# Performance work log

Measured on AMD Instinct MI355X. Metric: run time of the kernel, lower is better.

Reference implementation:

```python
import jax, jax.numpy as jnp
import numpy as np

N_TOKENS = 8192
TOP_K = 2
N_EXPERTS = 8
D_MODEL = 1024
D_FF = 2048
CAPACITY = 3072  # static per-expert buffer; mean load 2048, overflow prob ~0
FP8_MAX = 448.0


def setup_inputs() -> dict:
    key = jax.random.key(0)
    ks = jax.random.split(key, 6)
    x = jax.random.normal(ks[0], (N_TOKENS, D_MODEL), dtype=jnp.float32)
    expert_indices = jax.random.randint(ks[1], (N_TOKENS, TOP_K), 0, N_EXPERTS)
    expert_weights = jax.nn.softmax(jax.random.normal(ks[2], (N_TOKENS, TOP_K)), axis=-1).astype(jnp.float32)
    # trunc_normal init, std = sqrt(1/3)/sqrt(fan_in), fan_in = w.shape[1]
    std_in = (1.0 / 3.0) ** 0.5 / D_MODEL ** 0.5
    std_ff = (1.0 / 3.0) ** 0.5 / D_FF ** 0.5
    w1 = jnp.clip(jax.random.normal(ks[3], (N_EXPERTS, D_MODEL, D_FF), jnp.float32) * std_in, -2 * std_in, 2 * std_in)
    w2 = jnp.clip(jax.random.normal(ks[4], (N_EXPERTS, D_MODEL, D_FF), jnp.float32) * std_in, -2 * std_in, 2 * std_in)
    w3 = jnp.clip(jax.random.normal(ks[5], (N_EXPERTS, D_FF, D_MODEL), jnp.float32) * std_ff, -2 * std_ff, 2 * std_ff)
    return {"x": x, "expert_indices": expert_indices, "expert_weights": expert_weights,
            "w1": w1, "w2": w2, "w3": w3}


def reference(x, expert_indices, expert_weights, w1, w2, w3):
    n_tokens, d_model = x.shape
    top_k = expert_indices.shape[1]
    n_experts = w1.shape[0]

    # input fp8 scale (buffer fill_ in torch -> no grad)
    input_scale = jax.lax.stop_gradient(FP8_MAX / (jnp.max(jnp.abs(x)) + 1e-12) * 0.9)
    # w*_scale buffers are ones at inference (recalibration happens only randomly in training)
    w_scale = jnp.float32(1.0)

    # ---- dispatch: stable sort assignments by expert, compute slot positions ----
    flat_experts = expert_indices.reshape(-1)                       # [N*K]
    flat_weights = expert_weights.reshape(-1)                       # [N*K]
    token_indices = jnp.repeat(jnp.arange(n_tokens), top_k)         # [N*K]
    order = jnp.argsort(flat_experts)                               # stable sort
    sorted_experts = flat_experts[order]
    sorted_weights = flat_weights[order]
    sorted_tokens = token_indices[order]
    counts = jnp.bincount(flat_experts, length=n_experts)           # [E]
    seg_starts = jnp.cumsum(counts) - counts                        # [E]
    positions = jnp.arange(n_tokens * top_k) - seg_starts[sorted_experts]

    # scatter tokens into padded per-expert buffers [E, CAP, d]; OOB slots dropped
    padded = jnp.zeros((n_experts, CAPACITY, d_model), x.dtype)
    padded = padded.at[sorted_experts, positions].set(x[sorted_tokens], mode='drop')

    # ---- grouped SwiGLU with fp8-style quant/dequant scaling ----
    inp_scaled = jnp.clip(padded * input_scale, -FP8_MAX, FP8_MAX)  # [E, C, d]
    w1_s = jnp.clip(w1 * w_scale, -FP8_MAX, FP8_MAX)
    w2_s = jnp.clip(w2 * w_scale, -FP8_MAX, FP8_MAX)
    w3_s = jnp.clip(w3 * w_scale, -FP8_MAX, FP8_MAX)
    gate = jnp.einsum('ecd,edf->ecf', inp_scaled, w1_s) / (input_scale * w_scale)
    gate = jax.nn.silu(gate)
    value = jnp.einsum('ecd,edf->ecf', inp_scaled, w2_s) / (input_scale * w_scale)
    hidden = gate * value                                            # [E, C, f]
    # per-expert hidden amax (padded rows are zero -> same max as valid rows)
    hidden_amax = jnp.max(jnp.abs(hidden), axis=(1, 2))              # [E]
    hidden_scale = (FP8_MAX / (hidden_amax + 1e-12) * 0.9)[:, None, None]
    hidden_scaled = jnp.clip(hidden * hidden_scale, -FP8_MAX, FP8_MAX)
    out_padded = jnp.einsum('ecf,efd->ecd', hidden_scaled, w3_s) / (hidden_scale * w_scale)

    # ---- combine: gather per-assignment outputs, weight, scatter-add per token ----
    valid = positions < CAPACITY
    gathered = out_padded[sorted_experts, jnp.minimum(positions, CAPACITY - 1)]
    gathered = gathered * jnp.where(valid, sorted_weights, 0.0)[:, None]
    output = jnp.zeros((n_tokens, d_model), x.dtype).at[sorted_tokens].add(gathered)
    return output
```

## Files before the change

### kernel.cpp

```cpp
#include <hip/hip_runtime.h>

#define N_TOK   8192
#define TOPK    2
#define N_EXP   8
#define DM      1024
#define DFF     2048
#define CAP     3072

typedef __attribute__((ext_vector_type(8))) short bf16x8;
typedef __attribute__((ext_vector_type(4))) float f32x4;

__device__ __forceinline__ unsigned short f2bf(float x) {
    union { float f; unsigned u; } un; un.f = x;
    unsigned r = un.u + 0x7fffu + ((un.u >> 16) & 1u);
    return (unsigned short)(r >> 16);
}

__device__ __forceinline__ void glds16(const void* g, void* l) {
    __builtin_amdgcn_global_load_lds(
        (const __attribute__((address_space(1))) unsigned int*)g,
        (__attribute__((address_space(3))) unsigned int*)l, 16, 0, 0);
}

__global__ void cvt_x_kernel(const float4* __restrict__ x, ushort4* __restrict__ xb) {
    int i = blockIdx.x * 256 + threadIdx.x;
    float4 v = x[i];
    ushort4 o;
    o.x = f2bf(v.x); o.y = f2bf(v.y); o.z = f2bf(v.z); o.w = f2bf(v.w);
    xb[i] = o;
}

__global__ void transpose_cvt_kernel(const float* __restrict__ in, unsigned short* __restrict__ out,
                                     int R, int C) {
    __shared__ float tile[32][33];
    const int e = blockIdx.z;
    const int r0 = blockIdx.y * 32, c0 = blockIdx.x * 32;
    const float* src = in + ((size_t)e * R + r0) * C + c0;
    const int tx = threadIdx.x, ty = threadIdx.y;
#pragma unroll
    for (int i = 0; i < 4; i++)
        tile[ty + 8 * i][tx] = src[(size_t)(ty + 8 * i) * C + tx];
    __syncthreads();
    unsigned short* dst = out + ((size_t)e * C + c0) * R + r0;
#pragma unroll
    for (int i = 0; i < 4; i++) {
        int c = ty + 8 * i;
        dst[(size_t)c * R + tx] = f2bf(tile[tx][c]);
    }
}

__global__ void dispatch_kernel(const int* __restrict__ eidx, const float* __restrict__ ewt,
                                int* __restrict__ counts, int* __restrict__ row_token,
                                float* __restrict__ row_weight) {
    int i = blockIdx.x * 256 + threadIdx.x;
    if (i < N_TOK * TOPK) {
        int e = eidx[i];
        int pos = atomicAdd(&counts[e], 1);
        if (pos < CAP) {
            row_token[e * CAP + pos] = i >> 1;
            row_weight[e * CAP + pos] = ewt[i];
        }
    }
}

__global__ __launch_bounds__(256, 2)
void gemm1_kernel(const unsigned short* __restrict__ xb, const unsigned short* __restrict__ w1t,
                  const unsigned short* __restrict__ w2t, const int* __restrict__ counts,
                  const int* __restrict__ row_token, unsigned short* __restrict__ hidden) {
    const int e = blockIdx.z;
    const int r0 = blockIdx.y * 128;
    if (r0 >= counts[e]) return;
    const int f0 = blockIdx.x * 128;

    __shared__ unsigned short lA[128 * 32];
    __shared__ unsigned short lB1[128 * 32];
    __shared__ unsigned short lB2[128 * 32];

    const int t = threadIdx.x;
    const int lane = t & 63;
    const int wave = t >> 6;

    const int rstage = t >> 2;
    const int kbyte = (t & 3) * 16;

    const int tok0 = row_token[e * CAP + r0 + rstage];
    const int tok1 = row_token[e * CAP + r0 + 64 + rstage];
    const char* pA0 = (const char*)(xb + (size_t)tok0 * DM) + kbyte;
    const char* pA1 = (const char*)(xb + (size_t)tok1 * DM) + kbyte;
    const char* pB1a = (const char*)(w1t + ((size_t)e * DFF + f0 + rstage) * DM) + kbyte;
    const char* pB1b = pB1a + (size_t)64 * DM * 2;
    const char* pB2a = (const char*)(w2t + ((size_t)e * DFF + f0 + rstage) * DM) + kbyte;
    const char* pB2b = pB2a + (size_t)64 * DM * 2;

    char* lAp = (char*)lA + t * 16;
    char* lB1p = (char*)lB1 + t * 16;
    char* lB2p = (char*)lB2 + t * 16;

    const int mw = (wave & 1) * 64;
    const int nw = (wave >> 1) * 64;
    const int l15 = lane & 15;
    const int lq = lane >> 4;
    const unsigned short* aBase = lA + (mw + l15) * 32 + lq * 8;
    const unsigned short* b1Base = lB1 + (nw + l15) * 32 + lq * 8;
    const unsigned short* b2Base = lB2 + (nw + l15) * 32 + lq * 8;

    f32x4 accG[4][4];
    f32x4 accV[4][4];
#pragma unroll
    for (int i = 0; i < 4; i++)
#pragma unroll
        for (int j = 0; j < 4; j++) {
            accG[i][j] = (f32x4){0.f, 0.f, 0.f, 0.f};
            accV[i][j] = (f32x4){0.f, 0.f, 0.f, 0.f};
        }

    for (int k0 = 0; k0 < DM; k0 += 32) {
        glds16(pA0, lAp);            glds16(pA1, lAp + 4096);
        glds16(pB1a, lB1p);          glds16(pB1b, lB1p + 4096);
        glds16(pB2a, lB2p);          glds16(pB2b, lB2p + 4096);
        pA0 += 64; pA1 += 64; pB1a += 64; pB1b += 64; pB2a += 64; pB2b += 64;
        __syncthreads();

        bf16x8 a[4], b1[4], b2[4];
#pragma unroll
        for (int i = 0; i < 4; i++) {
            a[i]  = *(const bf16x8*)(aBase  + i * 512);
            b1[i] = *(const bf16x8*)(b1Base + i * 512);
            b2[i] = *(const bf16x8*)(b2Base + i * 512);
        }
#pragma unroll
        for (int i = 0; i < 4; i++)
#pragma unroll
            for (int j = 0; j < 4; j++) {
                accG[i][j] = __builtin_amdgcn_mfma_f32_16x16x32_bf16(a[i], b1[j], accG[i][j], 0, 0, 0);
                accV[i][j] = __builtin_amdgcn_mfma_f32_16x16x32_bf16(a[i], b2[j], accV[i][j], 0, 0, 0);
            }
        __syncthreads();
    }

    const size_t hbase = ((size_t)e * CAP + r0) * DFF + f0;
#pragma unroll
    for (int i = 0; i < 4; i++)
#pragma unroll
        for (int j = 0; j < 4; j++)
#pragma unroll
            for (int r = 0; r < 4; r++) {
                int m = mw + i * 16 + lq * 4 + r;
                int n = nw + j * 16 + l15;
                float g = accG[i][j][r];
                float v = accV[i][j][r];
                float h = (g / (1.f + __expf(-g))) * v;
                hidden[hbase + (size_t)m * DFF + n] = f2bf(h);
            }
}

__global__ __launch_bounds__(256, 2)
void gemm2_kernel(const unsigned short* __restrict__ hidden, const unsigned short* __restrict__ w3t,
                  const int* __restrict__ counts, const int* __restrict__ row_token,
                  const float* __restrict__ row_weight, float* __restrict__ out) {
    const int e = blockIdx.z;
    const int r0 = blockIdx.y * 128;
    if (r0 >= counts[e]) return;
    const int d0 = blockIdx.x * 128;

    __shared__ unsigned short lA[128 * 32];
    __shared__ unsigned short lB[128 * 32];

    const int t = threadIdx.x;
    const int lane = t & 63;
    const int wave = t >> 6;

    const int rstage = t >> 2;
    const int kbyte = (t & 3) * 16;

    const char* pA0 = (const char*)(hidden + ((size_t)e * CAP + r0 + rstage) * DFF) + kbyte;
    const char* pA1 = pA0 + (size_t)64 * DFF * 2;
    const char* pB0 = (const char*)(w3t + ((size_t)e * DM + d0 + rstage) * DFF) + kbyte;
    const char* pB1 = pB0 + (size_t)64 * DFF * 2;

    char* lAp = (char*)lA + t * 16;
    char* lBp = (char*)lB + t * 16;

    const int mw = (wave & 1) * 64;
    const int nw = (wave >> 1) * 64;
    const int l15 = lane & 15;
    const int lq = lane >> 4;
    const unsigned short* aBase = lA + (mw + l15) * 32 + lq * 8;
    const unsigned short* bBase = lB + (nw + l15) * 32 + lq * 8;

    f32x4 acc[4][4];
#pragma unroll
    for (int i = 0; i < 4; i++)
#pragma unroll
        for (int j = 0; j < 4; j++) acc[i][j] = (f32x4){0.f, 0.f, 0.f, 0.f};

    for (int k0 = 0; k0 < DFF; k0 += 32) {
        glds16(pA0, lAp);  glds16(pA1, lAp + 4096);
        glds16(pB0, lBp);  glds16(pB1, lBp + 4096);
        pA0 += 64; pA1 += 64; pB0 += 64; pB1 += 64;
        __syncthreads();

        bf16x8 a[4], b[4];
#pragma unroll
        for (int i = 0; i < 4; i++) {
            a[i] = *(const bf16x8*)(aBase + i * 512);
            b[i] = *(const bf16x8*)(bBase + i * 512);
        }
#pragma unroll
        for (int i = 0; i < 4; i++)
#pragma unroll
            for (int j = 0; j < 4; j++)
                acc[i][j] = __builtin_amdgcn_mfma_f32_16x16x32_bf16(a[i], b[j], acc[i][j], 0, 0, 0);
        __syncthreads();
    }

    const float* rw = row_weight + e * CAP + r0;
    const int* rt = row_token + e * CAP + r0;
#pragma unroll
    for (int i = 0; i < 4; i++)
#pragma unroll
        for (int r = 0; r < 4; r++) {
            int m = mw + i * 16 + lq * 4 + r;
            float w = rw[m];
            if (w != 0.f) {
                int tok = rt[m];
                float* orow = out + (size_t)tok * DM + d0 + nw + l15;
#pragma unroll
                for (int j = 0; j < 4; j++)
                    atomicAdd(orow + j * 16, acc[i][j][r] * w);
            }
        }
}

extern "C" void kernel_launch(void* const* d_in, const int* in_sizes, int n_in,
                              void* d_out, int out_size, void* d_ws, size_t ws_size,
                              hipStream_t stream) {
    const float* x = (const float*)d_in[0];
    const int* eidx = (const int*)d_in[1];
    const float* ewt = (const float*)d_in[2];
    const float* w1 = (const float*)d_in[3];
    const float* w2 = (const float*)d_in[4];
    const float* w3 = (const float*)d_in[5];
    float* out = (float*)d_out;

    char* ws = (char*)d_ws;
    size_t off = 0;
    auto alloc = [&](size_t b) { size_t o = off; off += (b + 255) & ~(size_t)255; return o; };
    int*   counts     = (int*)(ws + alloc(N_EXP * 4));
    int*   row_token  = (int*)(ws + alloc((size_t)N_EXP * CAP * 4));
    float* row_weight = (float*)(ws + alloc((size_t)N_EXP * CAP * 4));
    size_t hdr_end = off;
    unsigned short* xb  = (unsigned short*)(ws + alloc((size_t)N_TOK * DM * 2));
    unsigned short* w1t = (unsigned short*)(ws + alloc((size_t)N_EXP * DFF * DM * 2));
    unsigned short* w2t = (unsigned short*)(ws + alloc((size_t)N_EXP * DFF * DM * 2));
    unsigned short* w3t = (unsigned short*)(ws + alloc((size_t)N_EXP * DM * DFF * 2));
    unsigned short* hidden = (unsigned short*)(ws + alloc((size_t)N_EXP * CAP * DFF * 2));
    (void)ws_size; (void)in_sizes; (void)n_in;

    hipMemsetAsync(d_out, 0, (size_t)out_size * sizeof(float), stream);
    hipMemsetAsync(ws, 0, hdr_end, stream);

    cvt_x_kernel<<<(N_TOK * DM / 4) / 256, 256, 0, stream>>>((const float4*)x, (ushort4*)xb);
    transpose_cvt_kernel<<<dim3(DFF / 32, DM / 32, N_EXP), dim3(32, 8), 0, stream>>>(w1, w1t, DM, DFF);
    transpose_cvt_kernel<<<dim3(DFF / 32, DM / 32, N_EXP), dim3(32, 8), 0, stream>>>(w2, w2t, DM, DFF);
    transpose_cvt_kernel<<<dim3(DM / 32, DFF / 32, N_EXP), dim3(32, 8), 0, stream>>>(w3, w3t, DFF, DM);
    dispatch_kernel<<<(N_TOK * TOPK) / 256, 256, 0, stream>>>(eidx, ewt, counts, row_token, row_weight);

    gemm1_kernel<<<dim3(DFF / 128, CAP / 128, N_EXP), 256, 0, stream>>>(xb, w1t, w2t, counts, row_token, hidden);
    gemm2_kernel<<<dim3(DM / 128, CAP / 128, N_EXP), 256, 0, stream>>>(hidden, w3t, counts, row_token, row_weight, out);
}
```

Measured before the change: 655.9 us.

## Swizzle GEMM LDS tiles and vectorize weight transpose-convert kernels

Adds an XOR swizzle on the 16-byte chunk index for both the global-to-LDS staging and the MFMA fragment reads in both GEMMs. This is meant to remove LDS bank conflicts on the 64-byte row stride. Separately, the three weight transpose kernels become two launches using 64x64 tiles, float4 loads, bf16 conversion before the LDS stage and ushort4 stores, which cuts transpose memory traffic and launch count. The swizzle has to match exactly between writer and reader, or the results are wrong.

```diff
diff --git a/kernel.cpp b/kernel.cpp
--- a/kernel.cpp
+++ b/kernel.cpp
@@ -30,22 +30,42 @@
     xb[i] = o;
 }
 
-__global__ void transpose_cvt_kernel(const float* __restrict__ in, unsigned short* __restrict__ out,
-                                     int R, int C) {
-    __shared__ float tile[32][33];
-    const int e = blockIdx.z;
-    const int r0 = blockIdx.y * 32, c0 = blockIdx.x * 32;
-    const float* src = in + ((size_t)e * R + r0) * C + c0;
-    const int tx = threadIdx.x, ty = threadIdx.y;
-#pragma unroll
-    for (int i = 0; i < 4; i++)
-        tile[ty + 8 * i][tx] = src[(size_t)(ty + 8 * i) * C + tx];
+__global__ void transpose_cvt64_kernel(const float* __restrict__ inA, const float* __restrict__ inB,
+                                       unsigned short* __restrict__ outA, unsigned short* __restrict__ outB,
+                                       int R, int C) {
+    __shared__ unsigned short L[64][72];
+    const int z = blockIdx.z;
+    const float* in = (z & 8) ? inB : inA;
+    unsigned short* out = (z & 8) ? outB : outA;
+    const int e = z & 7;
+    const int r0 = blockIdx.y * 64, c0 = blockIdx.x * 64;
+    const int t = threadIdx.x;
+    const int rr = t >> 4;
+    const int cv = t & 15;
+    const float4* src = (const float4*)(in + ((size_t)e * R + r0) * C + c0);
+    const int c4 = C >> 2;
+#pragma unroll
+    for (int i = 0; i < 4; i++) {
+        int r = rr + 16 * i;
+        float4 v = src[(size_t)r * c4 + cv];
+        L[r][cv * 4 + 0] = f2bf(v.x);
+        L[r][cv * 4 + 1] = f2bf(v.y);
+        L[r][cv * 4 + 2] = f2bf(v.z);
+        L[r][cv * 4 + 3] = f2bf(v.w);
+    }
     __syncthreads();
     unsigned short* dst = out + ((size_t)e * C + c0) * R + r0;
+    const int cc = t >> 4;
+    const int rv = t & 15;
 #pragma unroll
     for (int i = 0; i < 4; i++) {
-        int c = ty + 8 * i;
-        dst[(size_t)c * R + tx] = f2bf(tile[tx][c]);
+        int c = cc + 16 * i;
+        ushort4 o;
+        o.x = L[rv * 4 + 0][c];
+        o.y = L[rv * 4 + 1][c];
+        o.z = L[rv * 4 + 2][c];
+        o.w = L[rv * 4 + 3][c];
+        *(ushort4*)(dst + (size_t)c * R + rv * 4) = o;
     }
 }
 
@@ -81,7 +101,8 @@
     const int wave = t >> 6;
 
     const int rstage = t >> 2;
-    const int kbyte = (t & 3) * 16;
+    const int cs = (t & 3) ^ ((rstage >> 1) & 3);
+    const int kbyte = cs * 16;
 
     const int tok0 = row_token[e * CAP + r0 + rstage];
     const int tok1 = row_token[e * CAP + r0 + 64 + rstage];
@@ -100,9 +121,10 @@
     const int nw = (wave >> 1) * 64;
     const int l15 = lane & 15;
     const int lq = lane >> 4;
-    const unsigned short* aBase = lA + (mw + l15) * 32 + lq * 8;
-    const unsigned short* b1Base = lB1 + (nw + l15) * 32 + lq * 8;
-    const unsigned short* b2Base = lB2 + (nw + l15) * 32 + lq * 8;
+    const int swz = (l15 >> 1) & 3;
+    const unsigned short* aBase  = lA  + (mw + l15) * 32 + ((lq ^ swz) * 8);
+    const unsigned short* b1Base = lB1 + (nw + l15) * 32 + ((lq ^ swz) * 8);
+    const unsigned short* b2Base = lB2 + (nw + l15) * 32 + ((lq ^ swz) * 8);
 
     f32x4 accG[4][4];
     f32x4 accV[4][4];
@@ -171,7 +193,8 @@
     const int wave = t >> 6;
 
     const int rstage = t >> 2;
-    const int kbyte = (t & 3) * 16;
+    const int cs = (t & 3) ^ ((rstage >> 1) & 3);
+    const int kbyte = cs * 16;
 
     const char* pA0 = (const char*)(hidden + ((size_t)e * CAP + r0 + rstage) * DFF) + kbyte;
     const char* pA1 = pA0 + (size_t)64 * DFF * 2;
@@ -185,8 +208,9 @@
     const int nw = (wave >> 1) * 64;
     const int l15 = lane & 15;
     const int lq = lane >> 4;
-    const unsigned short* aBase = lA + (mw + l15) * 32 + lq * 8;
-    const unsigned short* bBase = lB + (nw + l15) * 32 + lq * 8;
+    const int swz = (l15 >> 1) & 3;
+    const unsigned short* aBase = lA + (mw + l15) * 32 + ((lq ^ swz) * 8);
+    const unsigned short* bBase = lB + (nw + l15) * 32 + ((lq ^ swz) * 8);
 
     f32x4 acc[4][4];
 #pragma unroll
@@ -261,9 +285,8 @@
     hipMemsetAsync(ws, 0, hdr_end, stream);
 
     cvt_x_kernel<<<(N_TOK * DM / 4) / 256, 256, 0, stream>>>((const float4*)x, (ushort4*)xb);
-    transpose_cvt_kernel<<<dim3(DFF / 32, DM / 32, N_EXP), dim3(32, 8), 0, stream>>>(w1, w1t, DM, DFF);
-    transpose_cvt_kernel<<<dim3(DFF / 32, DM / 32, N_EXP), dim3(32, 8), 0, stream>>>(w2, w2t, DM, DFF);
-    transpose_cvt_kernel<<<dim3(DM / 32, DFF / 32, N_EXP), dim3(32, 8), 0, stream>>>(w3, w3t, DFF, DM);
+    transpose_cvt64_kernel<<<dim3(DFF / 64, DM / 64, 16), 256, 0, stream>>>(w1, w2, w1t, w2t, DM, DFF);
+    transpose_cvt64_kernel<<<dim3(DM / 64, DFF / 64, 8), 256, 0, stream>>>(w3, w3, w3t, w3t, DFF, DM);
     dispatch_kernel<<<(N_TOK * TOPK) / 256, 256, 0, stream>>>(eidx, ewt, counts, row_token, row_weight);
 
     gemm1_kernel<<<dim3(DFF / 128, CAP / 128, N_EXP), 256, 0, stream>>>(xb, w1t, w2t, counts, row_token, hidden);
```

After: 641.8 us. 2.1% less time.
